# Performance work log

Hardware: AMD Instinct MI355X
Metric: run time of the kernel (lower is better)

Reference implementation:

```python
import jax, jax.numpy as jnp
import numpy as np

HIDDEN = 896
N_HEADS = 14
N_KV = 2
HEAD_DIM = HIDDEN // N_HEADS  # 64
N_REP = N_HEADS // N_KV       # 7
ROPE_THETA = 1000000.0


def setup_inputs() -> dict:
    key = jax.random.key(0)
    ks = jax.random.split(key, 8)
    B, S = 2, 2048
    s = 0.02
    return {
        "hidden_states": jax.random.normal(ks[0], (B, S, HIDDEN), dtype=jnp.float32),
        "position_ids": jnp.broadcast_to(jnp.arange(S, dtype=jnp.int64), (B, S)),
        "Wq": jax.random.normal(ks[1], (HIDDEN, HIDDEN), dtype=jnp.float32) * s,
        "bq": jnp.zeros((HIDDEN,), dtype=jnp.float32),
        "Wk": jax.random.normal(ks[2], (N_KV * HEAD_DIM, HIDDEN), dtype=jnp.float32) * s,
        "bk": jnp.zeros((N_KV * HEAD_DIM,), dtype=jnp.float32),
        "Wv": jax.random.normal(ks[3], (N_KV * HEAD_DIM, HIDDEN), dtype=jnp.float32) * s,
        "bv": jnp.zeros((N_KV * HEAD_DIM,), dtype=jnp.float32),
        "Wo": jax.random.normal(ks[4], (HIDDEN, HIDDEN), dtype=jnp.float32) * s,
    }


def _rotate_half(x):
    x1, x2 = x[..., : HEAD_DIM // 2], x[..., HEAD_DIM // 2 :]
    return jnp.concatenate((-x2, x1), axis=-1)


def reference(hidden_states, position_ids, Wq, bq, Wk, bk, Wv, bv, Wo):
    B, S, _ = hidden_states.shape
    q = (hidden_states @ Wq.T + bq).reshape(B, S, N_HEADS, HEAD_DIM)
    k = (hidden_states @ Wk.T + bk).reshape(B, S, N_KV, HEAD_DIM)
    v = (hidden_states @ Wv.T + bv).reshape(B, S, N_KV, HEAD_DIM)

    # RoPE: cos/sin [B, S, 1, HEAD_DIM]
    inv_freq = 1.0 / (ROPE_THETA ** (jnp.arange(0, HEAD_DIM, 2, dtype=jnp.float32) / HEAD_DIM))
    freqs = position_ids.astype(jnp.float32)[..., None] * inv_freq  # [B,S,D/2]
    emb = jnp.concatenate((freqs, freqs), axis=-1)
    cos = jnp.cos(emb)[:, :, None, :]
    sin = jnp.sin(emb)[:, :, None, :]
    q = q * cos + _rotate_half(q) * sin
    k = k * cos + _rotate_half(k) * sin

    # [B, H, S, D]; repeat KV heads (GQA)
    q = q.transpose(0, 2, 1, 3)
    k = jnp.repeat(k.transpose(0, 2, 1, 3), N_REP, axis=1)
    v = jnp.repeat(v.transpose(0, 2, 1, 3), N_REP, axis=1)

    scale = 1.0 / np.sqrt(HEAD_DIM)
    scores = jnp.einsum("bhqd,bhkd->bhqk", q, k) * scale
    causal = jnp.tril(jnp.ones((S, S), dtype=bool))
    scores = jnp.where(causal[None, None, :, :], scores, jnp.finfo(scores.dtype).min)
    probs = jax.nn.softmax(scores, axis=-1)
    attn = jnp.einsum("bhqk,bhkd->bhqd", probs, v)  # [B,H,S,D]
    attn = attn.transpose(0, 2, 1, 3).reshape(B, S, HIDDEN)
    return attn @ Wo.T
```

## Files before the change

kernel.cpp:

```cpp
#include <hip/hip_runtime.h>

#define HID 896
#define NH 14
#define NKV 2
#define NREP 7
#define SEQ 2048
#define BT 2
#define NTOK (BT*SEQ)
#define CSCALE 0.18033688011112042f

typedef __attribute__((ext_vector_type(8))) short bf16x8;
typedef __attribute__((ext_vector_type(8))) unsigned short u16x8;
typedef __attribute__((ext_vector_type(4))) float fx4;
typedef __attribute__((ext_vector_type(4))) short s16x4;
typedef _Float16 f16x4 __attribute__((ext_vector_type(4)));
typedef __fp16 fp16x2 __attribute__((ext_vector_type(2)));

__device__ __forceinline__ unsigned short f2b(float x){
  union { float f; unsigned u; } a; a.f = x;
  unsigned r = a.u + 0x7FFFu + ((a.u >> 16) & 1u);
  return (unsigned short)(r >> 16);
}
__device__ __forceinline__ unsigned short f2h(float x){
  union { _Float16 h; unsigned short u; } a; a.h = (_Float16)x; return a.u;
}

__device__ __forceinline__ void gll16(const unsigned short* g, short* lds){
  __builtin_amdgcn_global_load_lds(
      (const __attribute__((address_space(1))) unsigned int*)(const void*)g,
      (__attribute__((address_space(3))) unsigned int*)(void*)lds, 16, 0, 0);
}

__global__ __launch_bounds__(256) void cvt_kernel(
    const float* __restrict__ s0, const float* __restrict__ s1,
    const float* __restrict__ s2, const float* __restrict__ s3,
    unsigned short* __restrict__ d0, unsigned short* __restrict__ d1,
    unsigned short* __restrict__ d2, unsigned short* __restrict__ d3,
    int c0, int c1, int c2, int c3,
    float2* __restrict__ tab)
{
  if (blockIdx.y == 4){
    for (int i = blockIdx.x*256 + threadIdx.x; i < SEQ*32; i += gridDim.x*256){
      int s = i >> 5, d = i & 31;
      float f = (float)s * exp2f(-(float)d * 0.62286151779138041f);
      float sv, cv; sincosf(f, &sv, &cv);
      tab[i] = make_float2(cv, sv);
    }
    return;
  }
  const float* s; unsigned short* d; int c;
  switch (blockIdx.y){
    case 0: s=s0; d=d0; c=c0; break;
    case 1: s=s1; d=d1; c=c1; break;
    case 2: s=s2; d=d2; c=c2; break;
    default: s=s3; d=d3; c=c3; break;
  }
  for (int i = (blockIdx.x*256 + threadIdx.x)*8; i < c; i += gridDim.x*2048){
    float4 a = *(const float4*)(s + i);
    float4 b = *(const float4*)(s + i + 4);
    u16x8 o;
    o[0]=f2b(a.x); o[1]=f2b(a.y); o[2]=f2b(a.z); o[3]=f2b(a.w);
    o[4]=f2b(b.x); o[5]=f2b(b.y); o[6]=f2b(b.z); o[7]=f2b(b.w);
    *(u16x8*)(d + i) = o;
  }
}

__global__ __launch_bounds__(256) void qkv_gemm_kernel(
    const float* __restrict__ Ahid, const unsigned short* __restrict__ Bw,
    const float* __restrict__ bq, const float* __restrict__ bk, const float* __restrict__ bv,
    const int* __restrict__ pos, const float2* __restrict__ tab,
    unsigned short* __restrict__ qo, unsigned short* __restrict__ ko,
    unsigned short* __restrict__ vt)
{
  __shared__ short As[2][64*64];
  __shared__ short Bs[2][128*64];
  const int tid = threadIdx.x;
  const int bm = blockIdx.x, bn = blockIdx.y;
  const int w = tid >> 6, l = tid & 63, l15 = l & 15, q4 = l >> 4;
  const int wm = w >> 1, wn = w & 1;
  const int lr = l >> 3;
  const int cbg = (l & 7) ^ lr;
  const int sw = l15 & 7;

  fx4 acc[2][4] = {};

  const float*          Ag = Ahid + (size_t)(bm*64)*HID;
  const unsigned short* Bg = Bw   + (size_t)(bn*128)*HID;

  float4 Areg[2][2];
  auto loadA = [&](int kt){
    const int kc = kt*64 + cbg*8;
#pragma unroll
    for (int p = 0; p < 2; p++){
      const float* src = Ag + (size_t)((p*4 + w)*8 + lr)*HID + kc;
      Areg[p][0] = *(const float4*)(src);
      Areg[p][1] = *(const float4*)(src + 4);
    }
  };
  auto storeA = [&](int buf){
#pragma unroll
    for (int p = 0; p < 2; p++){
      int c = p*4 + w;
      u16x8 o;
      o[0]=f2b(Areg[p][0].x); o[1]=f2b(Areg[p][0].y);
      o[2]=f2b(Areg[p][0].z); o[3]=f2b(Areg[p][0].w);
      o[4]=f2b(Areg[p][1].x); o[5]=f2b(Areg[p][1].y);
      o[6]=f2b(Areg[p][1].z); o[7]=f2b(Areg[p][1].w);
      *(u16x8*)&As[buf][c*512 + l*8] = o;
    }
  };
  auto issueB = [&](int kt, int buf){
    const int kc = kt*64 + cbg*8;
#pragma unroll
    for (int p = 0; p < 4; p++){
      int c = p*4 + w;
      gll16(Bg + (size_t)(c*8 + lr)*HID + kc, &Bs[buf][c*512]);
    }
  };

  issueB(0, 0);
  loadA(0);
  for (int kt = 0; kt < 14; kt++){
    const int cur = kt & 1;
    storeA(cur);
    if (kt < 13){
      issueB(kt+1, cur^1);
      loadA(kt+1);
    }
    asm volatile("s_waitcnt lgkmcnt(0)\n\ts_barrier" ::: "memory");
#pragma unroll
    for (int ks = 0; ks < 2; ks++){
      bf16x8 af[2], bf[4];
#pragma unroll
      for (int mt = 0; mt < 2; mt++){
        int r = wm*32 + mt*16 + l15;
        af[mt] = *(bf16x8*)&As[cur][r*64 + ((ks*4 + q4) ^ sw)*8];
      }
#pragma unroll
      for (int nt = 0; nt < 4; nt++){
        int r = wn*64 + nt*16 + l15;
        bf[nt] = *(bf16x8*)&Bs[cur][r*64 + ((ks*4 + q4) ^ sw)*8];
      }
#pragma unroll
      for (int mt = 0; mt < 2; mt++)
#pragma unroll
        for (int nt = 0; nt < 4; nt++)
          acc[mt][nt] = __builtin_amdgcn_mfma_f32_16x16x32_bf16(af[mt], bf[nt], acc[mt][nt], 0,0,0);
    }
    asm volatile("s_barrier" ::: "memory");
  }

  const int hu = bn*2 + wn;
  const float* bias; int kind, hloc;
  if (hu < NH)      { bias = bq + hu*64;      kind = 0; hloc = hu; }
  else if (hu < 16) { bias = bk + (hu-NH)*64; kind = 1; hloc = hu-NH; }
  else              { bias = bv + (hu-16)*64; kind = 2; hloc = hu-16; }
  float bl[4];
#pragma unroll
  for (int nt = 0; nt < 4; nt++) bl[nt] = bias[nt*16 + l15];

  if (kind == 2){
#pragma unroll
    for (int mt = 0; mt < 2; mt++)
#pragma unroll
      for (int j = 0; j < 4; j++){
        int grow = bm*64 + wm*32 + mt*16 + q4*4 + j;
        int b = grow >> 11, s = grow & (SEQ-1);
        int tile = s >> 6, key = s & 63;
        unsigned short* dst = vt + (size_t)(((b*NKV + hloc)*(SEQ/64) + tile)*4096);
#pragma unroll
        for (int nt = 0; nt < 4; nt++)
          dst[(nt*16 + l15)*64 + key] = f2h(acc[mt][nt][j] + bl[nt]);
      }
  } else {
    const float qs = (kind == 0) ? CSCALE : 1.0f;
#pragma unroll
    for (int mt = 0; mt < 2; mt++)
#pragma unroll
      for (int j = 0; j < 4; j++){
        int grow = bm*64 + wm*32 + mt*16 + q4*4 + j;
        int b = grow >> 11, s = grow & (SEQ-1);
        int p = pos[grow];
        const float2* rp = tab + p*32 + l15;
        float2 cs0 = rp[0], cs1 = rp[16];
        unsigned short* dst = (kind == 0)
            ? qo + ((size_t)(b*NH  + hloc)*SEQ + s)*64
            : ko + ((size_t)(b*NKV + hloc)*SEQ + s)*64;
        float x1 = acc[mt][0][j] + bl[0], x2 = acc[mt][2][j] + bl[2];
        float y1 = acc[mt][1][j] + bl[1], y2 = acc[mt][3][j] + bl[3];
        dst[l15]      = f2b((x1*cs0.x - x2*cs0.y)*qs);
        dst[16 + l15] = f2b((y1*cs1.x - y2*cs1.y)*qs);
        dst[32 + l15] = f2b((x2*cs0.x + x1*cs0.y)*qs);
        dst[48 + l15] = f2b((y2*cs1.x + y1*cs1.y)*qs);
      }
  }
}

__device__ __forceinline__ void smax_pv(
    const fx4* s, bool diag, int wl, int q4,
    float& m_run, float& l_run, fx4* o, const f16x4 vf[4][4])
{
  float tv[16];
#pragma unroll
  for (int tl = 0; tl < 4; tl++)
#pragma unroll
    for (int j = 0; j < 4; j++){
      float x = s[tl][j];
      if (diag && (tl*16 + q4*4 + j > wl)) x = -1e30f;
      tv[tl*4+j] = x;
    }
  float mx = tv[0];
#pragma unroll
  for (int i = 1; i < 16; i++) mx = fmaxf(mx, tv[i]);
  mx = fmaxf(mx, __shfl_xor(mx, 16));
  mx = fmaxf(mx, __shfl_xor(mx, 32));
  float mn = fmaxf(m_run, mx);
  float al = exp2f(m_run - mn);
  m_run = mn;
  float p[16], rs = 0.f;
#pragma unroll
  for (int i = 0; i < 16; i++){ p[i] = exp2f(tv[i] - mn); rs += p[i]; }
  rs += __shfl_xor(rs, 16);
  rs += __shfl_xor(rs, 32);
  l_run = l_run*al + rs;
#pragma unroll
  for (int nt = 0; nt < 4; nt++)
#pragma unroll
    for (int j = 0; j < 4; j++) o[nt][j] *= al;
  f16x4 pf[4];
#pragma unroll
  for (int tl = 0; tl < 4; tl++){
    union { f16x4 v; fp16x2 h[2]; } u;
    u.h[0] = __builtin_amdgcn_cvt_pkrtz(p[tl*4+0], p[tl*4+1]);
    u.h[1] = __builtin_amdgcn_cvt_pkrtz(p[tl*4+2], p[tl*4+3]);
    pf[tl] = u.v;
  }
#pragma unroll
  for (int nt = 0; nt < 4; nt++)
#pragma unroll
    for (int tl = 0; tl < 4; tl++)
      o[nt] = __builtin_amdgcn_mfma_f32_16x16x16f16(vf[nt][tl], pf[tl], o[nt], 0,0,0);
}

__global__ __launch_bounds__(512) void attn_kernel(
    const unsigned short* __restrict__ q, const unsigned short* __restrict__ k,
    const unsigned short* __restrict__ vt, unsigned short* __restrict__ ao)
{
  __shared__ short SB[8*64*72];

  const int tid = threadIdx.x;
  const int w = tid >> 6, l = tid & 63, l15 = l & 15, q4 = l >> 4;
  const int g = w >> 2, wi = w & 3;
  const int tlo = blockIdx.x, thi = 31 - tlo;
  const int h = blockIdx.y, b = blockIdx.z, kvh = h / NREP;
  const int wl = wi*16 + l15;

  const unsigned short* qbase = q + ((size_t)(b*NH + h)*SEQ)*64;
  const unsigned short* qpA = qbase + (size_t)(thi*64 + wl)*64;
  const unsigned short* qpB = qbase + (size_t)(tlo*64 + wl)*64;
  bf16x8 qA0 = *(const bf16x8*)(qpA + q4*8), qA1 = *(const bf16x8*)(qpA + 32 + q4*8);
  bf16x8 qB0 = *(const bf16x8*)(qpB + q4*8), qB1 = *(const bf16x8*)(qpB + 32 + q4*8);

  fx4 oA[4] = {}, oB[4] = {};
  float mA = -1e30f, lA = 0.f, mB = -1e30f, lB = 0.f;

  const unsigned short* kbase = k  + ((size_t)(b*NKV + kvh)*SEQ)*64;
  const unsigned short* vbase = vt + (size_t)((b*NKV + kvh)*(SEQ/64))*4096;

  const int P = (thi + 2) >> 1;

  u16x8 kreg[2], vreg[2];
#pragma unroll
  for (int p2 = 0; p2 < 2; p2++){
    int idx = p2*512 + tid, tile = idx >> 9, off = idx & 511;
    kreg[p2] = *(const u16x8*)(kbase + (size_t)tile*4096 + off*8);
    vreg[p2] = *(const u16x8*)(vbase + (size_t)tile*4096 + off*8);
  }
#pragma unroll
  for (int p2 = 0; p2 < 2; p2++){
    int idx = p2*512 + tid, tile = idx >> 9, off = idx & 511;
    int rr = off >> 3, g8 = off & 7;
    *(u16x8*)&SB[tile*4608 + rr*72 + g8*8] = kreg[p2];
    *(u16x8*)&SB[9216 + tile*4608 + rr*72 + g8*8] = vreg[p2];
  }

  for (int si = 0; si < P; si++){
    asm volatile("s_waitcnt lgkmcnt(0)\n\ts_barrier" ::: "memory");
    const int p = si & 1;
    const bool more = (si + 1 < P);

    if (more){
      const int k0n = 2*(si+1);
#pragma unroll
      for (int p2 = 0; p2 < 2; p2++){
        int idx = p2*512 + tid, tile = idx >> 9, off = idx & 511;
        int tk = k0n + tile; if (tk > thi) tk = thi;
        kreg[p2] = *(const u16x8*)(kbase + (size_t)tk*4096 + off*8);
        vreg[p2] = *(const u16x8*)(vbase + (size_t)tk*4096 + off*8);
      }
    }

    const int kt = 2*si + g;
    if (kt <= thi){
      const short* Kst = SB + p*18432 + g*4608;
      const short* Vtt = SB + p*18432 + 9216 + g*4608;
      bf16x8 kf0[4], kf1[4];
#pragma unroll
      for (int tl = 0; tl < 4; tl++){
        kf0[tl] = *(const bf16x8*)&Kst[(tl*16 + l15)*72 + q4*8];
        kf1[tl] = *(const bf16x8*)&Kst[(tl*16 + l15)*72 + 32 + q4*8];
      }
      f16x4 vf[4][4];
#pragma unroll
      for (int nt = 0; nt < 4; nt++)
#pragma unroll
        for (int tl = 0; tl < 4; tl++)
          vf[nt][tl] = *(const f16x4*)&Vtt[(nt*16 + l15)*72 + tl*16 + q4*4];

      {
        fx4 s[4] = {};
#pragma unroll
        for (int tl = 0; tl < 4; tl++){
          s[tl] = __builtin_amdgcn_mfma_f32_16x16x32_bf16(kf0[tl], qA0, s[tl], 0,0,0);
          s[tl] = __builtin_amdgcn_mfma_f32_16x16x32_bf16(kf1[tl], qA1, s[tl], 0,0,0);
        }
        smax_pv(s, kt == thi, wl, q4, mA, lA, oA, vf);
      }
      if (kt <= tlo){
        fx4 s[4] = {};
#pragma unroll
        for (int tl = 0; tl < 4; tl++){
          s[tl] = __builtin_amdgcn_mfma_f32_16x16x32_bf16(kf0[tl], qB0, s[tl], 0,0,0);
          s[tl] = __builtin_amdgcn_mfma_f32_16x16x32_bf16(kf1[tl], qB1, s[tl], 0,0,0);
        }
        smax_pv(s, kt == tlo, wl, q4, mB, lB, oB, vf);
      }
    }

    if (more){
      const int pn = (si & 1) ^ 1;
#pragma unroll
      for (int p2 = 0; p2 < 2; p2++){
        int idx = p2*512 + tid, tile = idx >> 9, off = idx & 511;
        int rr = off >> 3, g8 = off & 7;
        *(u16x8*)&SB[pn*18432 + tile*4608 + rr*72 + g8*8] = kreg[p2];
        *(u16x8*)&SB[pn*18432 + 9216 + tile*4608 + rr*72 + g8*8] = vreg[p2];
      }
    }
  }
  __syncthreads();

  float* F = (float*)SB;
  if (g == 1){
    float* fa = F + (((wi*2 + 0)*64 + l)*18);
#pragma unroll
    for (int nt = 0; nt < 4; nt++)
#pragma unroll
      for (int j = 0; j < 4; j++) fa[nt*4 + j] = oA[nt][j];
    fa[16] = mA; fa[17] = lA;
    float* fb = F + (((wi*2 + 1)*64 + l)*18);
#pragma unroll
    for (int nt = 0; nt < 4; nt++)
#pragma unroll
      for (int j = 0; j < 4; j++) fb[nt*4 + j] = oB[nt][j];
    fb[16] = mB; fb[17] = lB;
  }
  __syncthreads();
  if (g == 0){
    {
      const float* fa = F + (((wi*2 + 0)*64 + l)*18);
      float m1 = fa[16], l1 = fa[17];
      float mM = fmaxf(mA, m1);
      float a0 = exp2f(mA - mM), a1 = exp2f(m1 - mM);
      lA = lA*a0 + l1*a1;
#pragma unroll
      for (int nt = 0; nt < 4; nt++)
#pragma unroll
        for (int j = 0; j < 4; j++) oA[nt][j] = oA[nt][j]*a0 + fa[nt*4+j]*a1;
    }
    {
      const float* fb = F + (((wi*2 + 1)*64 + l)*18);
      float m1 = fb[16], l1 = fb[17];
      float mM = fmaxf(mB, m1);
      float a0 = exp2f(mB - mM), a1 = exp2f(m1 - mM);
      lB = lB*a0 + l1*a1;
#pragma unroll
      for (int nt = 0; nt < 4; nt++)
#pragma unroll
        for (int j = 0; j < 4; j++) oB[nt][j] = oB[nt][j]*a0 + fb[nt*4+j]*a1;
    }
    {
      float inv = 1.0f / lA;
      unsigned short* dst = ao + ((size_t)(b*SEQ + thi*64 + wl))*HID + h*64;
#pragma unroll
      for (int nt = 0; nt < 4; nt++){
        s16x4 ov;
        ov[0] = (short)f2b(oA[nt][0]*inv); ov[1] = (short)f2b(oA[nt][1]*inv);
        ov[2] = (short)f2b(oA[nt][2]*inv); ov[3] = (short)f2b(oA[nt][3]*inv);
        *(s16x4*)(dst + nt*16 + q4*4) = ov;
      }
    }
    {
      float inv = 1.0f / lB;
      unsigned short* dst = ao + ((size_t)(b*SEQ + tlo*64 + wl))*HID + h*64;
#pragma unroll
      for (int nt = 0; nt < 4; nt++){
        s16x4 ov;
        ov[0] = (short)f2b(oB[nt][0]*inv); ov[1] = (short)f2b(oB[nt][1]*inv);
        ov[2] = (short)f2b(oB[nt][2]*inv); ov[3] = (short)f2b(oB[nt][3]*inv);
        *(s16x4*)(dst + nt*16 + q4*4) = ov;
      }
    }
  }
}

__global__ __launch_bounds__(256) void out_gemm_kernel(
    const unsigned short* __restrict__ A, const unsigned short* __restrict__ Bw,
    float* __restrict__ out)
{
  __shared__ short As[2][64*64];
  __shared__ short Bs[2][128*64];
  const int tid = threadIdx.x;
  const int bm = blockIdx.x, bn = blockIdx.y;
  const int w = tid >> 6, l = tid & 63, l15 = l & 15, q4 = l >> 4;
  const int wm = w >> 1, wn = w & 1;
  const int lr = l >> 3;
  const int cbg = (l & 7) ^ lr;
  const int sw = l15 & 7;

  fx4 acc[2][4] = {};

  const unsigned short* Ag = A  + (size_t)(bm*64)*HID;
  const unsigned short* Bg = Bw + (size_t)(bn*128)*HID;

  auto issue = [&](int kt, int buf){
    const int kc = kt*64 + cbg*8;
#pragma unroll
    for (int p = 0; p < 2; p++){
      int c = p*4 + w;
      gll16(Ag + (size_t)(c*8 + lr)*HID + kc, &As[buf][c*512]);
    }
#pragma unroll
    for (int p = 0; p < 4; p++){
      int c = p*4 + w;
      gll16(Bg + (size_t)(c*8 + lr)*HID + kc, &Bs[buf][c*512]);
    }
  };

  issue(0, 0);
  for (int kt = 0; kt < 14; kt++){
    const int cur = kt & 1;
    if (kt < 13){
      issue(kt+1, cur^1);
      asm volatile("s_waitcnt vmcnt(6)\n\ts_barrier" ::: "memory");
    } else {
      asm volatile("s_waitcnt vmcnt(0)\n\ts_barrier" ::: "memory");
    }
#pragma unroll
    for (int ks = 0; ks < 2; ks++){
      bf16x8 af[2], bf[4];
#pragma unroll
      for (int mt = 0; mt < 2; mt++){
        int r = wm*32 + mt*16 + l15;
        af[mt] = *(bf16x8*)&As[cur][r*64 + ((ks*4 + q4) ^ sw)*8];
      }
#pragma unroll
      for (int nt = 0; nt < 4; nt++){
        int r = wn*64 + nt*16 + l15;
        bf[nt] = *(bf16x8*)&Bs[cur][r*64 + ((ks*4 + q4) ^ sw)*8];
      }
#pragma unroll
      for (int mt = 0; mt < 2; mt++)
#pragma unroll
        for (int nt = 0; nt < 4; nt++)
          acc[mt][nt] = __builtin_amdgcn_mfma_f32_16x16x32_bf16(af[mt], bf[nt], acc[mt][nt], 0,0,0);
    }
    asm volatile("s_barrier" ::: "memory");
  }

#pragma unroll
  for (int mt = 0; mt < 2; mt++)
#pragma unroll
    for (int j = 0; j < 4; j++){
      int grow = bm*64 + wm*32 + mt*16 + q4*4 + j;
      float* dst = out + (size_t)grow*HID + bn*128 + wn*64;
#pragma unroll
      for (int nt = 0; nt < 4; nt++)
        dst[nt*16 + l15] = acc[mt][nt][j];
    }
}

extern "C" void kernel_launch(void* const* d_in, const int* in_sizes, int n_in,
                              void* d_out, int out_size, void* d_ws, size_t ws_size,
                              hipStream_t stream)
{
  const float* hidden = (const float*)d_in[0];
  const int*   pos    = (const int*)d_in[1];
  const float* Wq = (const float*)d_in[2]; const float* bq = (const float*)d_in[3];
  const float* Wk = (const float*)d_in[4]; const float* bk = (const float*)d_in[5];
  const float* Wv = (const float*)d_in[6]; const float* bv = (const float*)d_in[7];
  const float* Wo = (const float*)d_in[8];

  unsigned short* qws   = (unsigned short*)d_ws;
  unsigned short* kws   = qws   + (size_t)BT*NH*SEQ*64;
  unsigned short* vtws  = kws   + (size_t)BT*NKV*SEQ*64;
  unsigned short* wqkv  = vtws  + (size_t)BT*NKV*SEQ*64;
  unsigned short* wo16  = wqkv  + (size_t)1152*HID;
  unsigned short* h16   = wo16  + (size_t)HID*HID;
  float2*         tab   = (float2*)(h16 + (size_t)NTOK*HID);

  const int nwq  = HID*HID;
  const int nwkv = 2*64*HID;

  cvt_kernel<<<dim3(448, 5), 256, 0, stream>>>(
      Wq, Wk, Wv, Wo,
      wqkv, wqkv + nwq, wqkv + nwq + nwkv, wo16,
      nwq, nwkv, nwkv, nwq, tab);

  qkv_gemm_kernel<<<dim3(NTOK/64, 9), 256, 0, stream>>>(
      hidden, wqkv, bq, bk, bv, pos, tab, qws, kws, vtws);

  attn_kernel<<<dim3(16, NH, BT), 512, 0, stream>>>(qws, kws, vtws, h16);

  out_gemm_kernel<<<dim3(NTOK/64, 7), 256, 0, stream>>>(h16, wo16, (float*)d_out);
}
```

Baseline: 170.9 us.

## Split attention KV range across two blocks and add a reduce kernel

Each query-tile pair's KV loop is split into two halves handled by separate blocks, which doubles the attention grid from 448 to 896 blocks to improve occupancy across CUs. Each block writes unnormalized fp32 partial outputs along with its running max and sum to workspace. A new reduce kernel then merges the two halves, normalizes, and writes bf16 output. In exchange, this adds an extra launch, fp32 partial traffic, and an assumption that workspace has room for the partials.

```diff
diff --git a/kernel.cpp b/kernel.cpp
--- a/kernel.cpp
+++ b/kernel.cpp
@@ -244,16 +244,22 @@
 
 __global__ __launch_bounds__(512) void attn_kernel(
     const unsigned short* __restrict__ q, const unsigned short* __restrict__ k,
-    const unsigned short* __restrict__ vt, unsigned short* __restrict__ ao)
+    const unsigned short* __restrict__ vt, float* __restrict__ part)
 {
   __shared__ short SB[8*64*72];
 
   const int tid = threadIdx.x;
   const int w = tid >> 6, l = tid & 63, l15 = l & 15, q4 = l >> 4;
   const int g = w >> 2, wi = w & 3;
-  const int tlo = blockIdx.x, thi = 31 - tlo;
+  const int pairx = blockIdx.x & 15, half = blockIdx.x >> 4;
+  const int tlo = pairx, thi = 31 - tlo;
   const int h = blockIdx.y, b = blockIdx.z, kvh = h / NREP;
   const int wl = wi*16 + l15;
+
+  const int P  = (thi + 2) >> 1;
+  const int Ph = (P + 1) >> 1;
+  const int s0 = half ? Ph : 0;
+  const int s1 = half ? P  : Ph;
 
   const unsigned short* qbase = q + ((size_t)(b*NH + h)*SEQ)*64;
   const unsigned short* qpA = qbase + (size_t)(thi*64 + wl)*64;
@@ -267,27 +273,29 @@
   const unsigned short* kbase = k  + ((size_t)(b*NKV + kvh)*SEQ)*64;
   const unsigned short* vbase = vt + (size_t)((b*NKV + kvh)*(SEQ/64))*4096;
 
-  const int P = (thi + 2) >> 1;
-
   u16x8 kreg[2], vreg[2];
 #pragma unroll
   for (int p2 = 0; p2 < 2; p2++){
     int idx = p2*512 + tid, tile = idx >> 9, off = idx & 511;
-    kreg[p2] = *(const u16x8*)(kbase + (size_t)tile*4096 + off*8);
-    vreg[p2] = *(const u16x8*)(vbase + (size_t)tile*4096 + off*8);
-  }
-#pragma unroll
-  for (int p2 = 0; p2 < 2; p2++){
-    int idx = p2*512 + tid, tile = idx >> 9, off = idx & 511;
-    int rr = off >> 3, g8 = off & 7;
-    *(u16x8*)&SB[tile*4608 + rr*72 + g8*8] = kreg[p2];
-    *(u16x8*)&SB[9216 + tile*4608 + rr*72 + g8*8] = vreg[p2];
-  }
-
-  for (int si = 0; si < P; si++){
+    int tk = 2*s0 + tile; if (tk > thi) tk = thi;
+    kreg[p2] = *(const u16x8*)(kbase + (size_t)tk*4096 + off*8);
+    vreg[p2] = *(const u16x8*)(vbase + (size_t)tk*4096 + off*8);
+  }
+  {
+    const int buf0 = s0 & 1;
+#pragma unroll
+    for (int p2 = 0; p2 < 2; p2++){
+      int idx = p2*512 + tid, tile = idx >> 9, off = idx & 511;
+      int rr = off >> 3, g8 = off & 7;
+      *(u16x8*)&SB[buf0*18432 + tile*4608 + rr*72 + g8*8] = kreg[p2];
+      *(u16x8*)&SB[buf0*18432 + 9216 + tile*4608 + rr*72 + g8*8] = vreg[p2];
+    }
+  }
+
+  for (int si = s0; si < s1; si++){
     asm volatile("s_waitcnt lgkmcnt(0)\n\ts_barrier" ::: "memory");
     const int p = si & 1;
-    const bool more = (si + 1 < P);
+    const bool more = (si + 1 < s1);
 
     if (more){
       const int k0n = 2*(si+1);
@@ -372,6 +380,7 @@
       float m1 = fa[16], l1 = fa[17];
       float mM = fmaxf(mA, m1);
       float a0 = exp2f(mA - mM), a1 = exp2f(m1 - mM);
+      mA = mM;
       lA = lA*a0 + l1*a1;
 #pragma unroll
       for (int nt = 0; nt < 4; nt++)
@@ -383,6 +392,7 @@
       float m1 = fb[16], l1 = fb[17];
       float mM = fmaxf(mB, m1);
       float a0 = exp2f(mB - mM), a1 = exp2f(m1 - mM);
+      mB = mM;
       lB = lB*a0 + l1*a1;
 #pragma unroll
       for (int nt = 0; nt < 4; nt++)
@@ -390,27 +400,51 @@
         for (int j = 0; j < 4; j++) oB[nt][j] = oB[nt][j]*a0 + fb[nt*4+j]*a1;
     }
     {
-      float inv = 1.0f / lA;
-      unsigned short* dst = ao + ((size_t)(b*SEQ + thi*64 + wl))*HID + h*64;
-#pragma unroll
-      for (int nt = 0; nt < 4; nt++){
-        s16x4 ov;
-        ov[0] = (short)f2b(oA[nt][0]*inv); ov[1] = (short)f2b(oA[nt][1]*inv);
-        ov[2] = (short)f2b(oA[nt][2]*inv); ov[3] = (short)f2b(oA[nt][3]*inv);
-        *(s16x4*)(dst + nt*16 + q4*4) = ov;
-      }
+      float* pp = part + ((((((size_t)half*BT + b)*NH + h)*16 + pairx)*2 + 0)*64 + wl)*68;
+#pragma unroll
+      for (int nt = 0; nt < 4; nt++)
+        *(fx4*)(pp + nt*16 + q4*4) = oA[nt];
+      if (q4 == 0){ pp[64] = mA; pp[65] = lA; }
     }
     {
-      float inv = 1.0f / lB;
-      unsigned short* dst = ao + ((size_t)(b*SEQ + tlo*64 + wl))*HID + h*64;
-#pragma unroll
-      for (int nt = 0; nt < 4; nt++){
-        s16x4 ov;
-        ov[0] = (short)f2b(oB[nt][0]*inv); ov[1] = (short)f2b(oB[nt][1]*inv);
-        ov[2] = (short)f2b(oB[nt][2]*inv); ov[3] = (short)f2b(oB[nt][3]*inv);
-        *(s16x4*)(dst + nt*16 + q4*4) = ov;
-      }
-    }
+      float* pp = part + ((((((size_t)half*BT + b)*NH + h)*16 + pairx)*2 + 1)*64 + wl)*68;
+#pragma unroll
+      for (int nt = 0; nt < 4; nt++)
+        *(fx4*)(pp + nt*16 + q4*4) = oB[nt];
+      if (q4 == 0){ pp[64] = mB; pp[65] = lB; }
+    }
+  }
+}
+
+__global__ __launch_bounds__(256) void attn_reduce_kernel(
+    const float* __restrict__ part, unsigned short* __restrict__ ao)
+{
+  const int pairx = blockIdx.x, h = blockIdx.y, b = blockIdx.z;
+  const int tid = threadIdx.x;
+  const int row2 = tid >> 1, hc = tid & 1;
+  const int strip = row2 >> 6, row = row2 & 63;
+  const int qt = strip ? pairx : (31 - pairx);
+
+  const float* p0 = part + (((((size_t)0*BT + b)*NH + h)*16 + pairx)*2 + strip)*64*68 + (size_t)row*68;
+  const float* p1 = part + (((((size_t)1*BT + b)*NH + h)*16 + pairx)*2 + strip)*64*68 + (size_t)row*68;
+  float m0 = p0[64], l0 = p0[65], m1 = p1[64], l1 = p1[65];
+  float mM = fmaxf(m0, m1);
+  float a0 = exp2f(m0 - mM), a1 = exp2f(m1 - mM);
+  float inv = 1.0f / (l0*a0 + l1*a1);
+  a0 *= inv; a1 *= inv;
+
+  unsigned short* dst = ao + ((size_t)(b*SEQ + qt*64 + row))*HID + h*64 + hc*32;
+  const float* q0 = p0 + hc*32;
+  const float* q1 = p1 + hc*32;
+#pragma unroll
+  for (int c = 0; c < 32; c += 4){
+    fx4 x0 = *(const fx4*)(q0 + c), x1 = *(const fx4*)(q1 + c);
+    s16x4 ov;
+    ov[0] = (short)f2b(x0[0]*a0 + x1[0]*a1);
+    ov[1] = (short)f2b(x0[1]*a0 + x1[1]*a1);
+    ov[2] = (short)f2b(x0[2]*a0 + x1[2]*a1);
+    ov[3] = (short)f2b(x0[3]*a0 + x1[3]*a1);
+    *(s16x4*)(dst + c) = ov;
   }
 }
 
@@ -508,6 +542,7 @@
   unsigned short* wo16  = wqkv  + (size_t)1152*HID;
   unsigned short* h16   = wo16  + (size_t)HID*HID;
   float2*         tab   = (float2*)(h16 + (size_t)NTOK*HID);
+  float*          part  = (float*)(tab + SEQ*32);
 
   const int nwq  = HID*HID;
   const int nwkv = 2*64*HID;
@@ -520,7 +555,9 @@
   qkv_gemm_kernel<<<dim3(NTOK/64, 9), 256, 0, stream>>>(
       hidden, wqkv, bq, bk, bv, pos, tab, qws, kws, vtws);
 
-  attn_kernel<<<dim3(16, NH, BT), 512, 0, stream>>>(qws, kws, vtws, h16);
+  attn_kernel<<<dim3(32, NH, BT), 512, 0, stream>>>(qws, kws, vtws, part);
+
+  attn_reduce_kernel<<<dim3(16, NH, BT), 256, 0, stream>>>(part, h16);
 
   out_gemm_kernel<<<dim3(NTOK/64, 7), 256, 0, stream>>>(h16, wo16, (float*)d_out);
 }
```

Measured after the change: 192.5 us. 1.13x slower.
